# Kernel optimization log

Measured on AMD Instinct MI355X. Metric: run time of the kernel, lower is better.

## Reference

```python
import jax, jax.numpy as jnp
import numpy as np

# dims: B nodes, K hops, N neighbors/node, channels/features per FeatTrans1d stage
B, K, N = 512, 2, 32
C0, F0 = 1, 512
C1, F1 = 4, 16
C2, F2 = 32, 1
NUM_CLASS = 40
EPS_BN = 1e-5
EPS_NORM = 1e-7


def softsign(x):
    return x / (1.0 + jnp.abs(x))


def sgnroot(x):
    return jnp.sign(x) * jnp.sqrt(jnp.abs(x))


def row_normalize(x):
    # normalize over axis 1 as in the torch code; NaN -> 0
    x = x / (jnp.abs(x).sum(axis=1, keepdims=True) + EPS_NORM)
    return jnp.where(jnp.isnan(x), 0.0, x)


def feature_adjacency(x, nb):
    # x: [B,C,F], nb: [B,N,C,F] -> fadj: [B,F,F]
    fadj = jnp.einsum('bcf,bncg->bfg', x, nb)
    fadj = fadj + jnp.swapaxes(fadj, -1, -2)
    return row_normalize(sgnroot(fadj))


def transform(x, fadj, W):
    # x: [B,C,F], fadj: [B,F,G], W: [D,C,G,E] -> [B,D,E]
    xg = jnp.einsum('bcf,bfg->bcg', x, fadj)
    return jnp.einsum('bcg,dcge->bde', xg, W)


def transform_nb(nb, fadj, W):
    # nb: [B,N,C,F], fadj: [B,F,G] (node i's fadj broadcast over its N neighbors)
    xg = jnp.einsum('bncf,bfg->bncg', nb, fadj)
    return jnp.einsum('bncg,dcge->bnde', xg, W)


def bn(x, gamma, beta, axes, ch_axis):
    # training-mode BatchNorm1d: batch stats per channel (biased variance)
    mean = x.mean(axes, keepdims=True)
    var = x.var(axes, keepdims=True)
    shape = [1] * x.ndim
    shape[ch_axis] = x.shape[ch_axis]
    return (x - mean) * jax.lax.rsqrt(var + EPS_BN) * gamma.reshape(shape) + beta.reshape(shape)


def setup_inputs() -> dict:
    key = jax.random.key(0)
    ks = jax.random.split(key, 8)
    x = jax.random.normal(ks[0], (B, C0, F0), jnp.float32)
    neighbor = jax.random.normal(ks[1], (B, K, N, C0, F0), jnp.float32)
    W1 = jax.random.normal(ks[2], (K, C1, C0, F0, F1), jnp.float32) * 0.05
    W2 = jax.random.normal(ks[3], (K, C2, C1, F1, F2), jnp.float32) * 0.1
    g1 = jnp.ones((K, C1), jnp.float32)
    b1 = jnp.zeros((K, C1), jnp.float32)
    g2 = jnp.ones((K, C2), jnp.float32)
    b2 = jnp.zeros((K, C2), jnp.float32)
    Wc1 = jax.random.normal(ks[4], (C2 * F2 * K, C2 * F2), jnp.float32) * 0.1
    bc1 = jnp.zeros((C2 * F2,), jnp.float32)
    Wc2 = jax.random.normal(ks[5], (C2 * F2, NUM_CLASS), jnp.float32) * 0.1
    bc2 = jnp.zeros((NUM_CLASS,), jnp.float32)
    return {"x": x, "neighbor": neighbor, "W1": W1, "g1": g1, "b1": b1,
            "W2": W2, "g2": g2, "b2": b2,
            "Wc1": Wc1, "bc1": bc1, "Wc2": Wc2, "bc2": bc2}


def reference(x, neighbor, W1, g1, b1, W2, g2, b2, Wc1, bc1, Wc2, bc2):
    outs = []
    for kk in range(K):  # fixed small hop count, structurally distinct weights
        nb_k = neighbor[:, kk]                      # [B,N,C0,F0]
        fadj1 = feature_adjacency(x, nb_k)          # [B,F0,F0]
        h = transform(x, fadj1, W1[kk])             # [B,C1,F1]
        nbh = transform_nb(nb_k, fadj1, W1[kk])     # [B,N,C1,F1]
        # BN over batch+feature dims for h; per-node BN over (N,F) for neighbors
        h = softsign(bn(h, g1[kk], b1[kk], (0, 2), 1))
        nbh = softsign(bn(nbh, g1[kk], b1[kk], (1, 3), 2))
        fadj2 = feature_adjacency(h, nbh)           # [B,F1,F1]
        h2 = transform(h, fadj2, W2[kk])            # [B,C2,F2]
        h2 = softsign(bn(h2, g2[kk], b2[kk], (0, 2), 1))
        outs.append(h2)
    x_khops = jnp.concatenate(outs, axis=1)         # [B, C2*K, F2]
    flat = x_khops.reshape(B, -1)                   # dropout is identity at eval
    hid = jax.nn.relu(flat @ Wc1 + bc1)
    return hid @ Wc2 + bc2                          # [B, NUM_CLASS]
```

## Files before the change

### kernel.cpp

```cpp
#include <hip/hip_runtime.h>
#include <hip/hip_bf16.h>

#define B_SZ 512
#define KHOP 2
#define NNB  32
#define F0   512
#define C1   4
#define F1   16
#define C2   32
#define NCLS 40

#define EPS_BN   1e-5f
#define EPS_NORM 1e-7f

typedef __attribute__((ext_vector_type(8))) short short8;
typedef __attribute__((ext_vector_type(4))) float f32x4;

__device__ __forceinline__ float softsignf(float v) { return v / (1.0f + fabsf(v)); }

__device__ __forceinline__ unsigned cvt_pk_bf16(float lo, float hi) {
    unsigned r;
    asm("v_cvt_pk_bf16_f32 %0, %1, %2" : "=v"(r) : "v"(lo), "v"(hi));
    return r;
}

__device__ __forceinline__ float vsqrtf(float x) {
    float r;
    asm("v_sqrt_f32 %0, %1" : "=v"(r) : "v"(x));
    return r;
}

__global__ __launch_bounds__(256) void k_prep(const float* __restrict__ W1,
                                              unsigned short* __restrict__ w1t,
                                              float* __restrict__ stats)
{
    const int idx = blockIdx.x * 256 + threadIdx.x;
    if (blockIdx.x == 0 && threadIdx.x < 144) stats[threadIdx.x] = 0.f;
    const int g  = idx & 511;
    const int de = (idx >> 9) & 63;
    const int kk = idx >> 15;
    const int d = de >> 4, e = de & 15;
    w1t[idx] = (unsigned short)cvt_pk_bf16(W1[((size_t)((kk * 4 + d) * 512) + g) * 16 + e], 0.f);
}

#define VT_BASE 32768
#define SMEM_MAIN 102400

__global__ __launch_bounds__(512, 2) void k_main(
    const float* __restrict__ xg_, const float* __restrict__ nbg,
    const unsigned short* __restrict__ w1t,
    const float* __restrict__ g1, const float* __restrict__ b1,
    float* __restrict__ h_raw, float* __restrict__ nbs_out,
    float* __restrict__ hsum)
{
    extern __shared__ char smem[];
    float* xl = (float*)(smem + 98304);
    float* sl = (float*)(smem + 100352);

    const int t = threadIdx.x;
    const int pair = blockIdx.x;
    const int b = pair >> 1, k = pair & 1;
    const int l = t & 63, w = t >> 6;
    const int m = w & 1, gsb = w >> 1;
    const int kol = l >> 4;
    const float* nbp = nbg + (size_t)pair * (NNB * F0);

    {
        const int oct = t & 63, ng = t >> 6;
        const int f0s = oct * 8;
        float sp0=0,sp1=0,sp2=0,sp3=0,sp4=0,sp5=0,sp6=0,sp7=0;
        #pragma unroll
        for (int ni = 0; ni < 4; ++ni) {
            const int n = ng * 4 + ni;
            float4 q0 = *(const float4*)(nbp + n * F0 + f0s);
            float4 q1 = *(const float4*)(nbp + n * F0 + f0s + 4);
            sp0 += q0.x; sp1 += q0.y; sp2 += q0.z; sp3 += q0.w;
            sp4 += q1.x; sp5 += q1.y; sp6 += q1.z; sp7 += q1.w;
            uint4 p;
            p.x = cvt_pk_bf16(q0.x, q0.y);
            p.y = cvt_pk_bf16(q0.z, q0.w);
            p.z = cvt_pk_bf16(q1.x, q1.y);
            p.w = cvt_pk_bf16(q1.z, q1.w);
            *(uint4*)(smem + n * 1024 + ((2 * f0s) ^ ((n & 7) << 4))) = p;
        }
        float* part = (float*)(smem + VT_BASE);
        *(float4*)(part + ng * 512 + f0s)     = make_float4(sp0, sp1, sp2, sp3);
        *(float4*)(part + ng * 512 + f0s + 4) = make_float4(sp4, sp5, sp6, sp7);
        xl[t] = xg_[b * F0 + t];
    }
    __syncthreads();
    {
        const float* part = (const float*)(smem + VT_BASE);
        float s = 0.f;
        #pragma unroll
        for (int p = 0; p < 8; ++p) s += part[p * 512 + t];
        sl[t] = s;
    }
    __syncthreads();

    const float xv = xl[t], sv = sl[t];
    float dS0 = 0.f, dS1 = 0.f, xS0 = 0.f, xS1 = 0.f;
    f32x4 acc[8];
    #pragma unroll
    for (int j = 0; j < 8; ++j) acc[j] = (f32x4){0.f, 0.f, 0.f, 0.f};

    const int swz = ((t >> 1) & 3) << 4;
    const int nA  = m * 16 + (l & 15);
    const int aSw = (nA & 7) << 4;

    #pragma unroll 1
    for (int strip = 0; strip < 16; ++strip) {
        const int f0 = strip * 32;
        char* vt = smem + VT_BASE + ((strip & 1) << 15);
        #pragma unroll
        for (int ko = 0; ko < 4; ++ko) {
            float4 xf0 = ((const float4*)xl)[(f0 >> 2) + ko * 2];
            float4 xf1 = ((const float4*)xl)[(f0 >> 2) + ko * 2 + 1];
            float4 sf0 = ((const float4*)sl)[(f0 >> 2) + ko * 2];
            float4 sf1 = ((const float4*)sl)[(f0 >> 2) + ko * 2 + 1];
            const float xf[8] = {xf0.x, xf0.y, xf0.z, xf0.w, xf1.x, xf1.y, xf1.z, xf1.w};
            const float sf[8] = {sf0.x, sf0.y, sf0.z, sf0.w, sf1.x, sf1.y, sf1.z, sf1.w};
            unsigned pk[4];
            float vprev = 0.f;
            #pragma unroll
            for (int i = 0; i < 8; ++i) {
                float r = sf[i] * xv + xf[i] * sv;
                float a = vsqrtf(fabsf(r));
                float v = copysignf(a, r);
                if (i & 1) {
                    dS1 += a; xS1 += xf[i] * v;
                    pk[i >> 1] = cvt_pk_bf16(vprev, v);
                } else {
                    dS0 += a; xS0 += xf[i] * v;
                    vprev = v;
                }
            }
            uint4 u; u.x = pk[0]; u.y = pk[1]; u.z = pk[2]; u.w = pk[3];
            *(uint4*)(vt + t * 64 + ((ko * 16) ^ swz)) = u;
        }
        __syncthreads();
        short8 afrag = *(const short8*)(smem + nA * 1024 +
                        ((f0 * 2 + kol * 16) ^ aSw));
        #pragma unroll
        for (int j = 0; j < 8; ++j) {
            const int g = gsb * 128 + j * 16 + (l & 15);
            short8 bfrag = *(const short8*)(vt + g * 64 +
                            ((kol * 16) ^ (((g >> 1) & 3) << 4)));
            acc[j] = __builtin_amdgcn_mfma_f32_16x16x32_bf16(afrag, bfrag, acc[j], 0, 0, 0);
        }
    }
    __syncthreads();

    {
        const float ia = 1.f / ((dS0 + dS1) + EPS_NORM);
        ((float*)(smem + VT_BASE))[t] = ia;
        ((float*)(smem + VT_BASE + 2048))[t] = (xS0 + xS1) * ia;
    }
    __syncthreads();

    {
        const float* invD = (const float*)(smem + VT_BASE);
        #pragma unroll
        for (int j = 0; j < 8; ++j) {
            const int g = gsb * 128 + j * 16 + (l & 15);
            const float iv = invD[g];
            #pragma unroll
            for (int r = 0; r < 4; ++r) {
                const int n = m * 16 + (l >> 4) * 4 + r;
                *(unsigned short*)(smem + n * 1024 + ((2 * g) ^ ((n & 7) << 4))) =
                    (unsigned short)cvt_pk_bf16(acc[j][r] * iv, 0.f);
            }
        }
    }
    __syncthreads();

    f32x4 acc3 = (f32x4){0.f, 0.f, 0.f, 0.f};
    f32x4 acch = (f32x4){0.f, 0.f, 0.f, 0.f};
    {
        const int de = gsb * 16 + (l & 15);
        const unsigned short* wtp = w1t + ((size_t)(k * 64 + de) * 512) + kol * 8;
        const float* xgx = (const float*)(smem + VT_BASE + 2048);
        #pragma unroll 2
        for (int ks = 0; ks < 16; ++ks) {
            short8 bfrag = *(const short8*)(wtp + ks * 32);
            short8 af = *(const short8*)(smem + nA * 1024 +
                        ((ks * 64 + kol * 16) ^ aSw));
            acc3 = __builtin_amdgcn_mfma_f32_16x16x32_bf16(af, bfrag, acc3, 0, 0, 0);
            if (m == 0) {
                short8 afh = {0, 0, 0, 0, 0, 0, 0, 0};
                if ((l & 15) == 0) {
                    float4 p0 = *(const float4*)(xgx + ks * 32 + kol * 8);
                    float4 p1 = *(const float4*)(xgx + ks * 32 + kol * 8 + 4);
                    uint4 pk;
                    pk.x = cvt_pk_bf16(p0.x, p0.y); pk.y = cvt_pk_bf16(p0.z, p0.w);
                    pk.z = cvt_pk_bf16(p1.x, p1.y); pk.w = cvt_pk_bf16(p1.z, p1.w);
                    __builtin_memcpy(&afh, &pk, 16);
                }
                acch = __builtin_amdgcn_mfma_f32_16x16x32_bf16(afh, bfrag, acch, 0, 0, 0);
            }
        }
    }

    float* redst = (float*)(smem + 36864);
    float* pnb   = (float*)(smem + 36928);
    {
        float vals[4];
        float s1 = 0.f, s2 = 0.f;
        #pragma unroll
        for (int r = 0; r < 4; ++r) {
            float v = acc3[r];
            vals[r] = v; s1 += v; s2 += v * v;
        }
        #pragma unroll
        for (int off = 32; off >= 1; off >>= 1) {
            s1 += __shfl_xor(s1, off);
            s2 += __shfl_xor(s2, off);
        }
        if (l == 0) { redst[w * 2] = s1; redst[w * 2 + 1] = s2; }
        __syncthreads();
        const float S1 = redst[w * 2]     + redst[(w ^ 1) * 2];
        const float S2 = redst[w * 2 + 1] + redst[(w ^ 1) * 2 + 1];
        const float mean = S1 * (1.f / 512.f);
        const float var  = S2 * (1.f / 512.f) - mean * mean;
        const float An   = g1[k * C1 + gsb] * rsqrtf(var + EPS_BN);
        const float Bn   = b1[k * C1 + gsb] - mean * An;
        float nbse = 0.f;
        #pragma unroll
        for (int r = 0; r < 4; ++r) nbse += softsignf(vals[r] * An + Bn);
        nbse += __shfl_xor(nbse, 16);
        nbse += __shfl_xor(nbse, 32);
        if (l < 16) pnb[m * 64 + gsb * 16 + l] = nbse;

        if (m == 0 && l < 16) {
            float hv = acch[0];
            h_raw[pair * 64 + gsb * 16 + l] = hv;
            float t1 = hv, t2 = hv * hv;
            #pragma unroll
            for (int off = 1; off <= 8; off <<= 1) {
                t1 += __shfl_xor(t1, off);
                t2 += __shfl_xor(t2, off);
            }
            if (l == 0) {
                atomicAdd(&hsum[k * 4 + gsb], t1);
                atomicAdd(&hsum[8 + k * 4 + gsb], t2);
            }
        }
    }
    __syncthreads();
    if (t < 64) nbs_out[pair * 64 + t] = pnb[t] + pnb[64 + t];
}

__global__ __launch_bounds__(256) void k_stage2(
    const float* __restrict__ h_rawg, const float* __restrict__ nbsg,
    const float* __restrict__ hsum,
    const float* __restrict__ g1, const float* __restrict__ b1,
    const float* __restrict__ W2,
    float* __restrict__ h2_raw, float* __restrict__ h2sum)
{
    __shared__ float hl[4][64], nl[4][64], fl[4][256], xg2l[4][64];
    const int t = threadIdx.x, wv = t >> 6, l = t & 63;
    const int pair = blockIdx.x * 4 + wv;
    const int k = pair & 1;
    const int d = l >> 4;
    {
        const float S1 = hsum[k * 4 + d], S2 = hsum[8 + k * 4 + d];
        const float mean = S1 * (1.f / 8192.f);
        const float var  = S2 * (1.f / 8192.f) - mean * mean;
        const float A = g1[k * 4 + d] * rsqrtf(var + EPS_BN);
        const float Bc = b1[k * 4 + d] - mean * A;
        float hv = h_rawg[pair * 64 + l];
        hl[wv][l] = softsignf(hv * A + Bc);
        nl[wv][l] = nbsg[pair * 64 + l];
    }
    __syncthreads();
    const int gcol = l & 15;
    float raw[4];
    #pragma unroll
    for (int j = 0; j < 4; ++j) {
        const int idx = l + 64 * j;
        const int f = idx >> 4;
        float a = 0.f;
        #pragma unroll
        for (int c = 0; c < 4; ++c) a += hl[wv][c * 16 + f] * nl[wv][c * 16 + gcol];
        raw[j] = a;
        fl[wv][idx] = a;
    }
    __syncthreads();
    float w4[4]; float Dp = 0.f;
    #pragma unroll
    for (int j = 0; j < 4; ++j) {
        const int idx = l + 64 * j;
        const int f = idx >> 4;
        float v = raw[j] + fl[wv][gcol * 16 + f];
        float a = vsqrtf(fabsf(v));
        Dp += a;
        w4[j] = copysignf(a, v);
    }
    Dp += __shfl_xor(Dp, 16);
    Dp += __shfl_xor(Dp, 32);
    const float invD = 1.f / (Dp + EPS_NORM);
    __syncthreads();
    #pragma unroll
    for (int j = 0; j < 4; ++j) fl[wv][l + 64 * j] = w4[j] * invD;
    __syncthreads();
    {
        const int c = l >> 4;
        float a = 0.f;
        #pragma unroll
        for (int f = 0; f < 16; ++f) a += hl[wv][c * 16 + f] * fl[wv][f * 16 + gcol];
        xg2l[wv][c * 16 + gcol] = a;
    }
    __syncthreads();
    if (l < 32) {
        const float* W2p = W2 + k * (C2 * C1 * F1) + l * (C1 * F1);
        float a = 0.f;
        #pragma unroll
        for (int i = 0; i < 64; ++i) a += xg2l[wv][i] * W2p[i];
        h2_raw[pair * 32 + l] = a;
        atomicAdd(&h2sum[k * 32 + l], a);
        atomicAdd(&h2sum[64 + k * 32 + l], a * a);
    }
}

__global__ __launch_bounds__(64) void k_cls(
    const float* __restrict__ h2_raw, const float* __restrict__ h2sum,
    const float* __restrict__ g2, const float* __restrict__ b2,
    const float* __restrict__ Wc1, const float* __restrict__ bc1,
    const float* __restrict__ Wc2, const float* __restrict__ bc2,
    float* __restrict__ out)
{
    __shared__ float flat[64];
    __shared__ float hid[32];
    const int b = blockIdx.x, l = threadIdx.x;
    const int k = l >> 5, d = l & 31;
    {
        const float S1 = h2sum[l], S2 = h2sum[64 + l];
        const float mean = S1 * (1.f / 512.f);
        const float var  = S2 * (1.f / 512.f) - mean * mean;
        const float A = g2[l] * rsqrtf(var + EPS_BN);
        const float Bc = b2[l] - mean * A;
        float v = h2_raw[(b * 2 + k) * 32 + d];
        flat[l] = softsignf(v * A + Bc);
    }
    __syncthreads();
    if (l < 32) {
        float a = bc1[l];
        #pragma unroll
        for (int i = 0; i < 64; ++i) a += flat[i] * Wc1[i * 32 + l];
        hid[l] = fmaxf(a, 0.f);
    }
    __syncthreads();
    if (l < NCLS) {
        float a = bc2[l];
        #pragma unroll
        for (int j = 0; j < 32; ++j) a += hid[j] * Wc2[j * NCLS + l];
        out[b * NCLS + l] = a;
    }
}

extern "C" void kernel_launch(void* const* d_in, const int* in_sizes, int n_in,
                              void* d_out, int out_size, void* d_ws, size_t ws_size,
                              hipStream_t stream)
{
    const float* x   = (const float*)d_in[0];
    const float* nbg = (const float*)d_in[1];
    const float* W1  = (const float*)d_in[2];
    const float* g1  = (const float*)d_in[3];
    const float* b1  = (const float*)d_in[4];
    const float* W2  = (const float*)d_in[5];
    const float* g2  = (const float*)d_in[6];
    const float* b2  = (const float*)d_in[7];
    const float* Wc1 = (const float*)d_in[8];
    const float* bc1 = (const float*)d_in[9];
    const float* Wc2 = (const float*)d_in[10];
    const float* bc2 = (const float*)d_in[11];
    float* out = (float*)d_out;
    float* ws  = (float*)d_ws;

    float* h_raw  = ws;
    float* nbs    = ws + 65536;
    float* h2_raw = ws + 131072;
    float* stats  = ws + 163840;
    float* hsum   = stats;
    float* h2sum  = stats + 16;
    unsigned short* w1t = (unsigned short*)h2_raw;

    hipLaunchKernelGGL(k_prep,   dim3(256),             dim3(256), 0, stream, W1, w1t, stats);
    hipLaunchKernelGGL(k_main,   dim3(B_SZ * KHOP),     dim3(512), SMEM_MAIN, stream,
                       x, nbg, w1t, g1, b1, h_raw, nbs, hsum);
    hipLaunchKernelGGL(k_stage2, dim3(B_SZ * KHOP / 4), dim3(256), 0, stream,
                       h_raw, nbs, hsum, g1, b1, W2, h2_raw, h2sum);
    hipLaunchKernelGGL(k_cls,    dim3(B_SZ),            dim3(64), 0, stream,
                       h2_raw, h2sum, g2, b2, Wc1, bc1, Wc2, bc2, out);
}
```

Measured before the change: 301.8 us.

## Generate fadj B-fragments in registers, drop LDS staging and double occupancy

The main loop now has each lane compute the sgnroot feature-adjacency values straight in MFMA B-fragment layout and feed them to the MFMA, instead of writing a double-buffered tile to shared memory and syncing every strip. This removes 64KB of LDS and 16 barriers per block, so launch bounds rise to 4 blocks per CU. In exchange each wave now covers both neighbor halves (two A fragments). The row-sum reductions move to cross-lane shuffles, and register pressure rises under the tighter occupancy bound.

```diff
diff --git a/kernel.cpp b/kernel.cpp
--- a/kernel.cpp
+++ b/kernel.cpp
@@ -43,10 +43,10 @@
     w1t[idx] = (unsigned short)cvt_pk_bf16(W1[((size_t)((kk * 4 + d) * 512) + g) * 16 + e], 0.f);
 }
 
-#define VT_BASE 32768
-#define SMEM_MAIN 102400
-
-__global__ __launch_bounds__(512, 2) void k_main(
+#define SCR_BASE 32768
+#define SMEM_MAIN 53248
+
+__global__ __launch_bounds__(512, 4) void k_main(
     const float* __restrict__ xg_, const float* __restrict__ nbg,
     const unsigned short* __restrict__ w1t,
     const float* __restrict__ g1, const float* __restrict__ b1,
@@ -54,15 +54,14 @@
     float* __restrict__ hsum)
 {
     extern __shared__ char smem[];
-    float* xl = (float*)(smem + 98304);
-    float* sl = (float*)(smem + 100352);
+    float* xl = (float*)(smem + 49152);
+    float* sl = (float*)(smem + 51200);
 
     const int t = threadIdx.x;
     const int pair = blockIdx.x;
     const int b = pair >> 1, k = pair & 1;
     const int l = t & 63, w = t >> 6;
-    const int m = w & 1, gsb = w >> 1;
-    const int kol = l >> 4;
+    const int gcol = l & 15, kol = l >> 4;
     const float* nbp = nbg + (size_t)pair * (NNB * F0);
 
     {
@@ -83,14 +82,14 @@
             p.w = cvt_pk_bf16(q1.z, q1.w);
             *(uint4*)(smem + n * 1024 + ((2 * f0s) ^ ((n & 7) << 4))) = p;
         }
-        float* part = (float*)(smem + VT_BASE);
+        float* part = (float*)(smem + SCR_BASE);
         *(float4*)(part + ng * 512 + f0s)     = make_float4(sp0, sp1, sp2, sp3);
         *(float4*)(part + ng * 512 + f0s + 4) = make_float4(sp4, sp5, sp6, sp7);
         xl[t] = xg_[b * F0 + t];
     }
     __syncthreads();
     {
-        const float* part = (const float*)(smem + VT_BASE);
+        const float* part = (const float*)(smem + SCR_BASE);
         float s = 0.f;
         #pragma unroll
         for (int p = 0; p < 8; ++p) s += part[p * 512 + t];
@@ -98,97 +97,106 @@
     }
     __syncthreads();
 
-    const float xv = xl[t], sv = sl[t];
-    float dS0 = 0.f, dS1 = 0.f, xS0 = 0.f, xS1 = 0.f;
-    f32x4 acc[8];
-    #pragma unroll
-    for (int j = 0; j < 8; ++j) acc[j] = (f32x4){0.f, 0.f, 0.f, 0.f};
-
-    const int swz = ((t >> 1) & 3) << 4;
-    const int nA  = m * 16 + (l & 15);
-    const int aSw = (nA & 7) << 4;
+    float xgr[4], sgr[4];
+    #pragma unroll
+    for (int j = 0; j < 4; ++j) {
+        const int g = w * 64 + j * 16 + gcol;
+        xgr[j] = xl[g];
+        sgr[j] = sl[g];
+    }
+    f32x4 acc[2][4];
+    #pragma unroll
+    for (int m2 = 0; m2 < 2; ++m2)
+        #pragma unroll
+        for (int j = 0; j < 4; ++j)
+            acc[m2][j] = (f32x4){0.f, 0.f, 0.f, 0.f};
+    float dS[4] = {0.f, 0.f, 0.f, 0.f};
+    float xS[4] = {0.f, 0.f, 0.f, 0.f};
+
+    const int nA0 = gcol, nA1 = 16 + gcol;
+    const int aSw0 = (nA0 & 7) << 4, aSw1 = (nA1 & 7) << 4;
 
     #pragma unroll 1
     for (int strip = 0; strip < 16; ++strip) {
         const int f0 = strip * 32;
-        char* vt = smem + VT_BASE + ((strip & 1) << 15);
-        #pragma unroll
-        for (int ko = 0; ko < 4; ++ko) {
-            float4 xf0 = ((const float4*)xl)[(f0 >> 2) + ko * 2];
-            float4 xf1 = ((const float4*)xl)[(f0 >> 2) + ko * 2 + 1];
-            float4 sf0 = ((const float4*)sl)[(f0 >> 2) + ko * 2];
-            float4 sf1 = ((const float4*)sl)[(f0 >> 2) + ko * 2 + 1];
-            const float xf[8] = {xf0.x, xf0.y, xf0.z, xf0.w, xf1.x, xf1.y, xf1.z, xf1.w};
-            const float sf[8] = {sf0.x, sf0.y, sf0.z, sf0.w, sf1.x, sf1.y, sf1.z, sf1.w};
+        const int fo = f0 + kol * 8;
+        float4 xq0 = *(const float4*)(xl + fo);
+        float4 xq1 = *(const float4*)(xl + fo + 4);
+        float4 sq0 = *(const float4*)(sl + fo);
+        float4 sq1 = *(const float4*)(sl + fo + 4);
+        const float xf[8] = {xq0.x, xq0.y, xq0.z, xq0.w, xq1.x, xq1.y, xq1.z, xq1.w};
+        const float sf[8] = {sq0.x, sq0.y, sq0.z, sq0.w, sq1.x, sq1.y, sq1.z, sq1.w};
+        short8 afrag0 = *(const short8*)(smem + nA0 * 1024 + ((f0 * 2 + kol * 16) ^ aSw0));
+        short8 afrag1 = *(const short8*)(smem + nA1 * 1024 + ((f0 * 2 + kol * 16) ^ aSw1));
+        #pragma unroll
+        for (int j = 0; j < 4; ++j) {
             unsigned pk[4];
             float vprev = 0.f;
             #pragma unroll
             for (int i = 0; i < 8; ++i) {
-                float r = sf[i] * xv + xf[i] * sv;
+                float r = xf[i] * sgr[j] + xgr[j] * sf[i];
                 float a = vsqrtf(fabsf(r));
                 float v = copysignf(a, r);
-                if (i & 1) {
-                    dS1 += a; xS1 += xf[i] * v;
-                    pk[i >> 1] = cvt_pk_bf16(vprev, v);
-                } else {
-                    dS0 += a; xS0 += xf[i] * v;
-                    vprev = v;
-                }
+                dS[j] += a;
+                xS[j] += xf[i] * v;
+                if (i & 1) pk[i >> 1] = cvt_pk_bf16(vprev, v);
+                else       vprev = v;
             }
-            uint4 u; u.x = pk[0]; u.y = pk[1]; u.z = pk[2]; u.w = pk[3];
-            *(uint4*)(vt + t * 64 + ((ko * 16) ^ swz)) = u;
-        }
-        __syncthreads();
-        short8 afrag = *(const short8*)(smem + nA * 1024 +
-                        ((f0 * 2 + kol * 16) ^ aSw));
-        #pragma unroll
-        for (int j = 0; j < 8; ++j) {
-            const int g = gsb * 128 + j * 16 + (l & 15);
-            short8 bfrag = *(const short8*)(vt + g * 64 +
-                            ((kol * 16) ^ (((g >> 1) & 3) << 4)));
-            acc[j] = __builtin_amdgcn_mfma_f32_16x16x32_bf16(afrag, bfrag, acc[j], 0, 0, 0);
-        }
-    }
-    __syncthreads();
-
-    {
-        const float ia = 1.f / ((dS0 + dS1) + EPS_NORM);
-        ((float*)(smem + VT_BASE))[t] = ia;
-        ((float*)(smem + VT_BASE + 2048))[t] = (xS0 + xS1) * ia;
-    }
-    __syncthreads();
-
-    {
-        const float* invD = (const float*)(smem + VT_BASE);
-        #pragma unroll
-        for (int j = 0; j < 8; ++j) {
-            const int g = gsb * 128 + j * 16 + (l & 15);
-            const float iv = invD[g];
+            short8 bfrag;
+            uint4 bp; bp.x = pk[0]; bp.y = pk[1]; bp.z = pk[2]; bp.w = pk[3];
+            __builtin_memcpy(&bfrag, &bp, 16);
+            acc[0][j] = __builtin_amdgcn_mfma_f32_16x16x32_bf16(afrag0, bfrag, acc[0][j], 0, 0, 0);
+            acc[1][j] = __builtin_amdgcn_mfma_f32_16x16x32_bf16(afrag1, bfrag, acc[1][j], 0, 0, 0);
+        }
+    }
+
+    float iv[4], xgxr[4];
+    #pragma unroll
+    for (int j = 0; j < 4; ++j) {
+        float d = dS[j], x = xS[j];
+        d += __shfl_xor(d, 16); d += __shfl_xor(d, 32);
+        x += __shfl_xor(x, 16); x += __shfl_xor(x, 32);
+        iv[j] = 1.f / (d + EPS_NORM);
+        xgxr[j] = x * iv[j];
+    }
+    __syncthreads();
+
+    float* xgx = (float*)(smem + SCR_BASE);
+    if (kol == 0) {
+        #pragma unroll
+        for (int j = 0; j < 4; ++j) xgx[w * 64 + j * 16 + gcol] = xgxr[j];
+    }
+    #pragma unroll
+    for (int m2 = 0; m2 < 2; ++m2)
+        #pragma unroll
+        for (int j = 0; j < 4; ++j) {
+            const int g = w * 64 + j * 16 + gcol;
             #pragma unroll
             for (int r = 0; r < 4; ++r) {
-                const int n = m * 16 + (l >> 4) * 4 + r;
+                const int n = m2 * 16 + kol * 4 + r;
                 *(unsigned short*)(smem + n * 1024 + ((2 * g) ^ ((n & 7) << 4))) =
-                    (unsigned short)cvt_pk_bf16(acc[j][r] * iv, 0.f);
+                    (unsigned short)cvt_pk_bf16(acc[m2][j][r] * iv[j], 0.f);
             }
         }
-    }
-    __syncthreads();
-
+    __syncthreads();
+
+    const int m3 = w & 1, dsb = w >> 1;
+    const int nA = m3 * 16 + gcol;
+    const int aSw = (nA & 7) << 4;
     f32x4 acc3 = (f32x4){0.f, 0.f, 0.f, 0.f};
     f32x4 acch = (f32x4){0.f, 0.f, 0.f, 0.f};
     {
-        const int de = gsb * 16 + (l & 15);
+        const int de = dsb * 16 + gcol;
         const unsigned short* wtp = w1t + ((size_t)(k * 64 + de) * 512) + kol * 8;
-        const float* xgx = (const float*)(smem + VT_BASE + 2048);
         #pragma unroll 2
         for (int ks = 0; ks < 16; ++ks) {
             short8 bfrag = *(const short8*)(wtp + ks * 32);
             short8 af = *(const short8*)(smem + nA * 1024 +
                         ((ks * 64 + kol * 16) ^ aSw));
             acc3 = __builtin_amdgcn_mfma_f32_16x16x32_bf16(af, bfrag, acc3, 0, 0, 0);
-            if (m == 0) {
+            if (m3 == 0) {
                 short8 afh = {0, 0, 0, 0, 0, 0, 0, 0};
-                if ((l & 15) == 0) {
+                if (gcol == 0) {
                     float4 p0 = *(const float4*)(xgx + ks * 32 + kol * 8);
                     float4 p1 = *(const float4*)(xgx + ks * 32 + kol * 8 + 4);
                     uint4 pk;
@@ -201,8 +209,8 @@
         }
     }
 
-    float* redst = (float*)(smem + 36864);
-    float* pnb   = (float*)(smem + 36928);
+    float* redst = (float*)(smem + 34816);
+    float* pnb   = (float*)(smem + 34880);
     {
         float vals[4];
         float s1 = 0.f, s2 = 0.f;
@@ -222,18 +230,18 @@
         const float S2 = redst[w * 2 + 1] + redst[(w ^ 1) * 2 + 1];
         const float mean = S1 * (1.f / 512.f);
         const float var  = S2 * (1.f / 512.f) - mean * mean;
-        const float An   = g1[k * C1 + gsb] * rsqrtf(var + EPS_BN);
-        const float Bn   = b1[k * C1 + gsb] - mean * An;
+        const float An   = g1[k * C1 + dsb] * rsqrtf(var + EPS_BN);
+        const float Bn   = b1[k * C1 + dsb] - mean * An;
         float nbse = 0.f;
         #pragma unroll
         for (int r = 0; r < 4; ++r) nbse += softsignf(vals[r] * An + Bn);
         nbse += __shfl_xor(nbse, 16);
         nbse += __shfl_xor(nbse, 32);
-        if (l < 16) pnb[m * 64 + gsb * 16 + l] = nbse;
-
-        if (m == 0 && l < 16) {
+        if (l < 16) pnb[m3 * 64 + dsb * 16 + l] = nbse;
+
+        if (m3 == 0 && l < 16) {
             float hv = acch[0];
-            h_raw[pair * 64 + gsb * 16 + l] = hv;
+            h_raw[pair * 64 + dsb * 16 + l] = hv;
             float t1 = hv, t2 = hv * hv;
             #pragma unroll
             for (int off = 1; off <= 8; off <<= 1) {
@@ -241,8 +249,8 @@
                 t2 += __shfl_xor(t2, off);
             }
             if (l == 0) {
-                atomicAdd(&hsum[k * 4 + gsb], t1);
-                atomicAdd(&hsum[8 + k * 4 + gsb], t2);
+                atomicAdd(&hsum[k * 4 + dsb], t1);
+                atomicAdd(&hsum[8 + k * 4 + dsb], t2);
             }
         }
     }
```

New measurement: 262.1 us. -13.1%, faster.
